# Optimization experiments

Measured on AMD Instinct MI355X. Metric: run time of the kernel, lower is better.

## Reference

```python
import jax, jax.numpy as jnp
import numpy as np
import math

HID = 128
NH = 8
HD = HID // NH
NL = 3
CLIP = 10.0
EPS = 1e-5

def _ln(x, g, b):
    mu = jnp.mean(x, axis=-1, keepdims=True)
    var = jnp.var(x, axis=-1, keepdims=True)
    return (x - mu) * jax.lax.rsqrt(var + EPS) * g + b

def _layer(h, e_bias1, e_gate2, g1, b1, wh, g2, b2, w1, w2):
    B, N, _ = h.shape
    h_in = h
    hn = _ln(h, g1, b1)
    qkv = hn @ wh                                   # (B,N,3H)
    q, k, v = jnp.split(qkv, 3, axis=-1)
    q = q.reshape(B, N, NH, HD).transpose(0, 2, 1, 3)  # (B,nh,N,hd)
    k = k.reshape(B, N, NH, HD).transpose(0, 2, 1, 3)
    v = v.reshape(B, N, NH, HD).transpose(0, 2, 1, 3)
    att = jnp.einsum('bhid,bhjd->bhij', q, k) * (1.0 / math.sqrt(HD))
    att = jax.nn.softmax(att + e_bias1, axis=-1) * e_gate2
    y = jnp.einsum('bhij,bhjd->bhid', att, v)
    y = y.transpose(0, 2, 1, 3).reshape(B, N, HID)
    z = _ln(y + h_in, g2, b2)
    mlp = jax.nn.relu(z @ w1) @ w2
    return mlp + y

def setup_inputs() -> dict:
    key = jax.random.key(0)
    ks = jax.random.split(key, 9)
    d = {
        'node_features': jax.random.normal(ks[0], (16, 256, 2), jnp.float32),
        'edge_features': jax.random.normal(ks[1], (16, 256, 256, 1), jnp.float32),
        'Wn': jax.random.normal(ks[2], (2, HID), jnp.float32) * 0.5,
        'We_in': jax.random.normal(ks[3], (1, HID), jnp.float32) * 0.1,
        'ln1_g': jnp.ones((NL, HID), jnp.float32),
        'ln1_b': jnp.zeros((NL, HID), jnp.float32),
        'Wh': jax.random.normal(ks[4], (NL, HID, 3 * HID), jnp.float32) * (1.0 / math.sqrt(HID)),
        'We': jax.random.normal(ks[5], (NL, HID, 2 * NH), jnp.float32) * (1.0 / math.sqrt(HID)),
        'ln2_g': jnp.ones((NL, HID), jnp.float32),
        'ln2_b': jnp.zeros((NL, HID), jnp.float32),
        'W1': jax.random.normal(ks[6], (NL, HID, 4 * HID), jnp.float32) * (1.0 / math.sqrt(HID)),
        'W2': jax.random.normal(ks[7], (NL, 4 * HID, HID), jnp.float32) * (1.0 / math.sqrt(4 * HID)),
        'Wdec': jax.random.normal(ks[8], (HID, 1), jnp.float32) * (1.0 / math.sqrt(HID)),
    }
    return d

def reference(node_features, edge_features, Wn, We_in, ln1_g, ln1_b, Wh, We, ln2_g, ln2_b, W1, W2, Wdec):
    h = node_features @ Wn                              # (B,N,H)
    e = edge_features @ We_in                           # (B,N,N,H)
    for i in range(NL):
        ee = e @ We[i]                                  # (B,N,N,2*nh)
        ee = ee.transpose(0, 3, 1, 2)                   # (B,2*nh,N,N)
        e1, e2 = ee[:, :NH], ee[:, NH:]
        h = _layer(h, e1, e2, ln1_g[i], ln1_b[i], Wh[i], ln2_g[i], ln2_b[i], W1[i], W2[i])
    out = h @ Wdec                                      # (B,N,1)
    out = CLIP * jnp.tanh(out / math.sqrt(HID))
    return out
```

## Files before the change

### kernel.cpp

```cpp
#include <hip/hip_runtime.h>
#include <math.h>

#define HID 128
#define NHEAD 8
#define NL 3
#define NS 256
#define ROWS 4096

typedef __attribute__((ext_vector_type(8))) short bf16x8;
typedef __attribute__((ext_vector_type(4))) float f32x4;

__device__ __forceinline__ float us2f(unsigned short s) { return __uint_as_float(((unsigned)s) << 16); }
__device__ __forceinline__ unsigned short f2b(float f) {
    unsigned u = __float_as_uint(f);
    return (unsigned short)((u + 0x7fff + ((u >> 16) & 1)) >> 16);
}

__global__ __launch_bounds__(256) void k_prep(
    const float* __restrict__ Wh, const float* __restrict__ W1, const float* __restrict__ W2,
    const float* __restrict__ We_in, const float* __restrict__ We,
    const float* __restrict__ nf, const float* __restrict__ Wn,
    const float* __restrict__ ln1g, const float* __restrict__ ln1b,
    unsigned short* __restrict__ WhH, unsigned short* __restrict__ WhL,
    unsigned short* __restrict__ W1H, unsigned short* __restrict__ W1L,
    unsigned short* __restrict__ W2H, unsigned short* __restrict__ W2L,
    unsigned short* __restrict__ AH, unsigned short* __restrict__ AL,
    float* __restrict__ sbuf, float* __restrict__ h)
{
    int b = blockIdx.x, t = threadIdx.x;
    if (b >= 529) {
        int idx4 = (b - 529) * 256 + t;
        int r = idx4 >> 5, c4 = (idx4 & 31) * 4;
        float n0 = nf[2 * r], n1 = nf[2 * r + 1];
        float4 w0 = *(const float4*)&Wn[c4];
        float4 w1 = *(const float4*)&Wn[HID + c4];
        float v[4] = {n0 * w0.x + n1 * w1.x, n0 * w0.y + n1 * w1.y,
                      n0 * w0.z + n1 * w1.z, n0 * w0.w + n1 * w1.w};
        *(float4*)&h[idx4 * 4] = *(float4*)v;
        float s = v[0] + v[1] + v[2] + v[3];
        float s2 = v[0]*v[0] + v[1]*v[1] + v[2]*v[2] + v[3]*v[3];
        s  += __shfl_xor(s, 1);  s  += __shfl_xor(s, 2);  s  += __shfl_xor(s, 4);
        s  += __shfl_xor(s, 8);  s  += __shfl_xor(s, 16);
        s2 += __shfl_xor(s2, 1); s2 += __shfl_xor(s2, 2); s2 += __shfl_xor(s2, 4);
        s2 += __shfl_xor(s2, 8); s2 += __shfl_xor(s2, 16);
        float mu  = s * (1.f / HID);
        float var = s2 * (1.f / HID) - mu * mu;
        float inv = rsqrtf(var + 1e-5f);
        unsigned short hi4[4], lo4[4];
#pragma unroll
        for (int j = 0; j < 4; ++j) {
            int c = c4 + j;
            float o = (v[j] - mu) * inv * ln1g[c] + ln1b[c];
            hi4[j] = f2b(o); lo4[j] = f2b(o - us2f(hi4[j]));
        }
        *(uint2*)&AH[(long)r * HID + c4] = *(const uint2*)hi4;
        *(uint2*)&AL[(long)r * HID + c4] = *(const uint2*)lo4;
        return;
    }
    if (b == 528) {
        if (t < NL * 2 * NHEAD) {
            int l = t / (2 * NHEAD), j = t % (2 * NHEAD);
            float acc = 0.f;
            for (int c = 0; c < HID; ++c)
                acc += We_in[c] * We[(long)(l * HID + c) * (2 * NHEAD) + j];
            sbuf[t] = acc;
        }
        return;
    }
    const float* S; unsigned short *OH, *OL; int K, N, kt, nt;
    if (b < 144) {
        int l = b / 48, rem = b % 48; kt = rem & 3; nt = rem >> 2; K = 128; N = 384;
        S = Wh + (long)l * 128 * 384; OH = WhH + (long)l * 384 * 128; OL = WhL + (long)l * 384 * 128;
    } else if (b < 336) {
        int b2 = b - 144; int l = b2 / 64, rem = b2 % 64; kt = rem & 3; nt = rem >> 2; K = 128; N = 512;
        S = W1 + (long)l * 128 * 512; OH = W1H + (long)l * 512 * 128; OL = W1L + (long)l * 512 * 128;
    } else {
        int b2 = b - 336; int l = b2 / 64, rem = b2 % 64; kt = rem & 15; nt = rem >> 4; K = 512; N = 128;
        S = W2 + (long)l * 512 * 128; OH = W2H + (long)l * 128 * 512; OL = W2L + (long)l * 128 * 512;
    }
    __shared__ float sm[32][33];
    int i0 = t >> 5, j = t & 31;
#pragma unroll
    for (int p = 0; p < 4; ++p) {
        int i = i0 + p * 8;
        sm[i][j] = S[(long)(kt * 32 + i) * N + nt * 32 + j];
    }
    __syncthreads();
#pragma unroll
    for (int p = 0; p < 4; ++p) {
        int n = i0 + p * 8;
        float v = sm[j][n];
        unsigned short hh = f2b(v);
        long o = (long)(nt * 32 + n) * K + kt * 32 + j;
        OH[o] = hh; OL[o] = f2b(v - us2f(hh));
    }
}

__global__ __launch_bounds__(256) void k_fgemm(
    const unsigned short* __restrict__ AH, const unsigned short* __restrict__ AL,
    const unsigned short* __restrict__ WH, const unsigned short* __restrict__ WL,
    unsigned short* __restrict__ Ch, unsigned short* __restrict__ Cl)
{
    __shared__ unsigned short sAh[64 * 136], sAl[64 * 136];
    __shared__ unsigned short sWh[64 * 136], sWl[64 * 136];
    int t = threadIdx.x;
    int row0 = blockIdx.y * 64, col0 = blockIdx.x * 64;

#pragma unroll
    for (int p = 0; p < 4; ++p) {
        int rr = (t >> 4) + p * 16, ck = t & 15;
        *(uint4*)&sWh[rr * 136 + ck * 8] = *(const uint4*)&WH[(long)(col0 + rr) * 128 + ck * 8];
        *(uint4*)&sWl[rr * 136 + ck * 8] = *(const uint4*)&WL[(long)(col0 + rr) * 128 + ck * 8];
        *(uint4*)&sAh[rr * 136 + ck * 8] = *(const uint4*)&AH[(long)(row0 + rr) * 128 + ck * 8];
        *(uint4*)&sAl[rr * 136 + ck * 8] = *(const uint4*)&AL[(long)(row0 + rr) * 128 + ck * 8];
    }
    __syncthreads();

    int w = t >> 6, lane = t & 63;
    int m = lane & 15, quad = lane >> 4;
    f32x4 acc[4];
#pragma unroll
    for (int i = 0; i < 4; ++i) acc[i] = (f32x4){0.f, 0.f, 0.f, 0.f};
#pragma unroll
    for (int c = 0; c < 4; ++c) {
        bf16x8 ah = *(const bf16x8*)&sAh[(w * 16 + m) * 136 + c * 32 + quad * 8];
        bf16x8 al = *(const bf16x8*)&sAl[(w * 16 + m) * 136 + c * 32 + quad * 8];
#pragma unroll
        for (int nt = 0; nt < 4; ++nt) {
            bf16x8 wh = *(const bf16x8*)&sWh[(nt * 16 + m) * 136 + c * 32 + quad * 8];
            bf16x8 wl = *(const bf16x8*)&sWl[(nt * 16 + m) * 136 + c * 32 + quad * 8];
            acc[nt] = __builtin_amdgcn_mfma_f32_16x16x32_bf16(ah, wh, acc[nt], 0, 0, 0);
            acc[nt] = __builtin_amdgcn_mfma_f32_16x16x32_bf16(ah, wl, acc[nt], 0, 0, 0);
            acc[nt] = __builtin_amdgcn_mfma_f32_16x16x32_bf16(al, wh, acc[nt], 0, 0, 0);
        }
    }
#pragma unroll
    for (int nt = 0; nt < 4; ++nt) {
        unsigned short hi4[4], lo4[4];
#pragma unroll
        for (int r = 0; r < 4; ++r) {
            float v = acc[nt][r];
            hi4[r] = f2b(v); lo4[r] = f2b(v - us2f(hi4[r]));
        }
        long o = (long)(col0 + nt * 16 + m) * ROWS + row0 + w * 16 + quad * 4;
        *(uint2*)&Ch[o] = *(const uint2*)hi4;
        *(uint2*)&Cl[o] = *(const uint2*)lo4;
    }
}

__global__ __launch_bounds__(512, 1) void k_mlp(
    const float* __restrict__ y, const float* __restrict__ h,
    const float* __restrict__ g, const float* __restrict__ b,
    const float* __restrict__ lng, const float* __restrict__ lnb,
    const unsigned short* __restrict__ W1H_, const unsigned short* __restrict__ W1L_,
    const unsigned short* __restrict__ W2H_, const unsigned short* __restrict__ W2L_,
    float* __restrict__ hout,
    unsigned short* __restrict__ AHo, unsigned short* __restrict__ ALo,
    const float* __restrict__ Wdec, float* __restrict__ out)
{
    __shared__ __align__(16) unsigned short sAh[16 * 136], sAl[16 * 136];
    __shared__ __align__(16) unsigned short sHh[16 * 520], sHl[16 * 520];
    int t = threadIdx.x;
    int row0 = blockIdx.x * 16;
    int w = t >> 6, lane = t & 63;
    int m = lane & 15, quad = lane >> 4;

    const unsigned short* w1h = W1H_ + (long)(w * 64 + m) * 128 + quad * 8;
    const unsigned short* w1l = W1L_ + (long)(w * 64 + m) * 128 + quad * 8;
    bf16x8 p1h[4], p1l[4];
#pragma unroll
    for (int nt = 0; nt < 4; ++nt) {
        p1h[nt] = *(const bf16x8*)&w1h[nt * 16 * 128];
        p1l[nt] = *(const bf16x8*)&w1l[nt * 16 * 128];
    }

    {
        int row = t >> 5, cb = (t & 31) * 4;
        float4 a4 = *(const float4*)&y[(long)(row0 + row) * HID + cb];
        float4 b4 = *(const float4*)&h[(long)(row0 + row) * HID + cb];
        float v[4] = {a4.x + b4.x, a4.y + b4.y, a4.z + b4.z, a4.w + b4.w};
        float s = v[0] + v[1] + v[2] + v[3];
        float s2 = v[0]*v[0] + v[1]*v[1] + v[2]*v[2] + v[3]*v[3];
        s  += __shfl_xor(s, 1);  s  += __shfl_xor(s, 2);  s  += __shfl_xor(s, 4);
        s  += __shfl_xor(s, 8);  s  += __shfl_xor(s, 16);
        s2 += __shfl_xor(s2, 1); s2 += __shfl_xor(s2, 2); s2 += __shfl_xor(s2, 4);
        s2 += __shfl_xor(s2, 8); s2 += __shfl_xor(s2, 16);
        float mu  = s * (1.f / HID);
        float var = s2 * (1.f / HID) - mu * mu;
        float inv = rsqrtf(var + 1e-5f);
        unsigned short hi4[4], lo4[4];
#pragma unroll
        for (int j = 0; j < 4; ++j) {
            int c = cb + j;
            float o = (v[j] - mu) * inv * g[c] + b[c];
            hi4[j] = f2b(o); lo4[j] = f2b(o - us2f(hi4[j]));
        }
        *(uint2*)&sAh[row * 136 + cb] = *(const uint2*)hi4;
        *(uint2*)&sAl[row * 136 + cb] = *(const uint2*)lo4;
    }
    __syncthreads();

    f32x4 acc1[4];
#pragma unroll
    for (int i = 0; i < 4; ++i) acc1[i] = (f32x4){0.f, 0.f, 0.f, 0.f};
#pragma unroll
    for (int c = 0; c < 4; ++c) {
        bf16x8 ah = *(const bf16x8*)&sAh[m * 136 + c * 32 + quad * 8];
        bf16x8 al = *(const bf16x8*)&sAl[m * 136 + c * 32 + quad * 8];
#pragma unroll
        for (int nt = 0; nt < 4; ++nt) {
            bf16x8 wh = (c == 0) ? p1h[nt] : *(const bf16x8*)&w1h[nt * 16 * 128 + c * 32];
            bf16x8 wl = (c == 0) ? p1l[nt] : *(const bf16x8*)&w1l[nt * 16 * 128 + c * 32];
            acc1[nt] = __builtin_amdgcn_mfma_f32_16x16x32_bf16(wh, ah, acc1[nt], 0, 0, 0);
            acc1[nt] = __builtin_amdgcn_mfma_f32_16x16x32_bf16(wh, al, acc1[nt], 0, 0, 0);
            acc1[nt] = __builtin_amdgcn_mfma_f32_16x16x32_bf16(wl, ah, acc1[nt], 0, 0, 0);
        }
    }
#pragma unroll
    for (int nt = 0; nt < 4; ++nt) {
        unsigned short hi4[4], lo4[4];
#pragma unroll
        for (int r = 0; r < 4; ++r) {
            float v = fmaxf(acc1[nt][r], 0.f);
            hi4[r] = f2b(v);
            lo4[r] = f2b(v - us2f(hi4[r]));
        }
        int kk = w * 64 + nt * 16 + quad * 4;
        *(uint2*)&sHh[m * 520 + kk] = *(const uint2*)hi4;
        *(uint2*)&sHl[m * 520 + kk] = *(const uint2*)lo4;
    }

    const unsigned short* w2h = W2H_ + (long)(w * 16 + m) * 512 + quad * 8;
    const unsigned short* w2l = W2L_ + (long)(w * 16 + m) * 512 + quad * 8;
    bf16x8 p2h = *(const bf16x8*)w2h;
    bf16x8 p2l = *(const bf16x8*)w2l;
    __syncthreads();

    f32x4 acc2 = (f32x4){0.f, 0.f, 0.f, 0.f};
#pragma unroll
    for (int c = 0; c < 16; ++c) {
        bf16x8 ah = *(const bf16x8*)&sHh[m * 520 + c * 32 + quad * 8];
        bf16x8 al = *(const bf16x8*)&sHl[m * 520 + c * 32 + quad * 8];
        bf16x8 wh = (c == 0) ? p2h : *(const bf16x8*)&w2h[c * 32];
        bf16x8 wl = (c == 0) ? p2l : *(const bf16x8*)&w2l[c * 32];
        acc2 = __builtin_amdgcn_mfma_f32_16x16x32_bf16(ah, wh, acc2, 0, 0, 0);
        acc2 = __builtin_amdgcn_mfma_f32_16x16x32_bf16(ah, wl, acc2, 0, 0, 0);
        acc2 = __builtin_amdgcn_mfma_f32_16x16x32_bf16(al, wh, acc2, 0, 0, 0);
    }
    __syncthreads();
    float* ht = (float*)&sHh[0];
#pragma unroll
    for (int r = 0; r < 4; ++r) {
        int row = quad * 4 + r;
        int col = w * 16 + m;
        float v = acc2[r] + y[(long)(row0 + row) * HID + col];
        hout[(long)(row0 + row) * HID + col] = v;
        ht[row * 132 + col] = v;
    }
    __syncthreads();
    if (Wdec) {
        if (t < 256) {
            int row = t >> 4, sub = t & 15;
            float vv[8];
            *(float4*)&vv[0] = *(const float4*)&ht[row * 132 + sub * 8];
            *(float4*)&vv[4] = *(const float4*)&ht[row * 132 + sub * 8 + 4];
            float a = 0.f;
#pragma unroll
            for (int j = 0; j < 8; ++j) a += vv[j] * Wdec[sub * 8 + j];
            a += __shfl_xor(a, 1); a += __shfl_xor(a, 2); a += __shfl_xor(a, 4); a += __shfl_xor(a, 8);
            if (sub == 0) out[row0 + row] = 10.f * tanhf(a * 0.08838834764831845f);
        }
    } else {
        int row = t >> 5, cb = (t & 31) * 4;
        float v[4];
        v[0] = ht[row * 132 + cb];     v[1] = ht[row * 132 + cb + 1];
        v[2] = ht[row * 132 + cb + 2]; v[3] = ht[row * 132 + cb + 3];
        float s = v[0] + v[1] + v[2] + v[3];
        float s2 = v[0]*v[0] + v[1]*v[1] + v[2]*v[2] + v[3]*v[3];
        s  += __shfl_xor(s, 1);  s  += __shfl_xor(s, 2);  s  += __shfl_xor(s, 4);
        s  += __shfl_xor(s, 8);  s  += __shfl_xor(s, 16);
        s2 += __shfl_xor(s2, 1); s2 += __shfl_xor(s2, 2); s2 += __shfl_xor(s2, 4);
        s2 += __shfl_xor(s2, 8); s2 += __shfl_xor(s2, 16);
        float mu  = s * (1.f / HID);
        float var = s2 * (1.f / HID) - mu * mu;
        float inv = rsqrtf(var + 1e-5f);
        unsigned short hi4[4], lo4[4];
#pragma unroll
        for (int j = 0; j < 4; ++j) {
            int c = cb + j;
            float o = (v[j] - mu) * inv * lng[c] + lnb[c];
            hi4[j] = f2b(o); lo4[j] = f2b(o - us2f(hi4[j]));
        }
        *(uint2*)&AHo[(long)(row0 + row) * HID + cb] = *(const uint2*)hi4;
        *(uint2*)&ALo[(long)(row0 + row) * HID + cb] = *(const uint2*)lo4;
    }
}

#define PAS 268
#define KQS 20
__global__ __launch_bounds__(256) void k_attn(
    const unsigned short* __restrict__ qkvH, const unsigned short* __restrict__ qkvL,
    const float* __restrict__ ef, const float* __restrict__ sbuf,
    int layer, float* __restrict__ y)
{
    __shared__ unsigned short Kh[NS * KQS], Kl[NS * KQS];
    __shared__ unsigned short Qh[64 * KQS], Ql[64 * KQS];
    __shared__ unsigned short Vh[16 * PAS], Vl[16 * PAS];
    __shared__ unsigned short Pa[4][16 * PAS];
    int bid = blockIdx.x;
    int q4 = bid & 3, hh = (bid >> 2) & 7, bb = bid >> 5;
    int t = threadIdx.x;
    {
        int d = t >> 4, kc = (t & 15) * 16;
        long base = (long)ROWS * (HID + hh * 16 + d) + bb * NS + kc;
        long vbase = base + (long)ROWS * 128;
        union { uint4 u[2]; unsigned short s[16]; } KH, KL, VH, VL;
        KH.u[0] = *(const uint4*)&qkvH[base];      KH.u[1] = *(const uint4*)&qkvH[base + 8];
        KL.u[0] = *(const uint4*)&qkvL[base];      KL.u[1] = *(const uint4*)&qkvL[base + 8];
        VH.u[0] = *(const uint4*)&qkvH[vbase];     VH.u[1] = *(const uint4*)&qkvH[vbase + 8];
        VL.u[0] = *(const uint4*)&qkvL[vbase];     VL.u[1] = *(const uint4*)&qkvL[vbase + 8];
#pragma unroll
        for (int j = 0; j < 16; ++j) {
            Kh[(kc + j) * KQS + d] = KH.s[j];
            Kl[(kc + j) * KQS + d] = KL.s[j];
        }
#pragma unroll
        for (int j = 0; j < 4; ++j) {
            *(uint2*)&Vh[d * PAS + kc + j * 4] = *(const uint2*)&VH.s[j * 4];
            *(uint2*)&Vl[d * PAS + kc + j * 4] = *(const uint2*)&VL.s[j * 4];
        }
    }
    {
        int d = t >> 4, rc = (t & 15) * 4;
        long qb = (long)ROWS * (hh * 16 + d) + bb * NS + q4 * 64 + rc;
        union { uint2 u; unsigned short s[4]; } QH, QL;
        QH.u = *(const uint2*)&qkvH[qb];
        QL.u = *(const uint2*)&qkvL[qb];
#pragma unroll
        for (int j = 0; j < 4; ++j) {
            Qh[(rc + j) * KQS + d] = QH.s[j];
            Ql[(rc + j) * KQS + d] = QL.s[j];
        }
    }
    __syncthreads();
    int w = t >> 6, lane = t & 63;
    int m = lane & 15, quad = lane >> 4;
    float s1  = sbuf[layer * 16 + hh];
    float s2g = sbuf[layer * 16 + NHEAD + hh];
    unsigned short* Paw = Pa[w];

    bf16x8 qh = (bf16x8){0,0,0,0,0,0,0,0}, ql = qh;
    if (quad < 2) {
        qh = *(const bf16x8*)&Qh[(w * 16 + m) * KQS + quad * 8];
        ql = *(const bf16x8*)&Ql[(w * 16 + m) * KQS + quad * 8];
    }
    f32x4 sc[16];
#pragma unroll
    for (int ct = 0; ct < 16; ++ct) {
        bf16x8 kh = (bf16x8){0,0,0,0,0,0,0,0}, kl = kh;
        if (quad < 2) {
            kh = *(const bf16x8*)&Kh[(ct * 16 + m) * KQS + quad * 8];
            kl = *(const bf16x8*)&Kl[(ct * 16 + m) * KQS + quad * 8];
        }
        f32x4 a = (f32x4){0.f, 0.f, 0.f, 0.f};
        a = __builtin_amdgcn_mfma_f32_16x16x32_bf16(qh, kh, a, 0, 0, 0);
        a = __builtin_amdgcn_mfma_f32_16x16x32_bf16(qh, kl, a, 0, 0, 0);
        a = __builtin_amdgcn_mfma_f32_16x16x32_bf16(ql, kh, a, 0, 0, 0);
        sc[ct] = a;
    }
    int baserow = q4 * 64 + w * 16 + quad * 4;
    float s[4] = {0.f, 0.f, 0.f, 0.f};
#pragma unroll
    for (int ct = 0; ct < 16; ++ct) {
#pragma unroll
        for (int r = 0; r < 4; ++r) {
            float e = ef[((long)(bb * NS + baserow + r)) * NS + ct * 16 + m];
            float p = __expf(sc[ct][r] * 0.25f + e * s1);
            s[r] += p;
            Paw[(quad * 4 + r) * PAS + ct * 16 + m] = f2b(p * e);
        }
    }
    float inv[4];
#pragma unroll
    for (int r = 0; r < 4; ++r) {
        float ss = s[r];
        ss += __shfl_xor(ss, 1); ss += __shfl_xor(ss, 2);
        ss += __shfl_xor(ss, 4); ss += __shfl_xor(ss, 8);
        inv[r] = s2g / ss;
    }
    f32x4 acc = (f32x4){0.f, 0.f, 0.f, 0.f};
#pragma unroll
    for (int sft = 0; sft < 8; ++sft) {
        bf16x8 pf = *(const bf16x8*)&Paw[m * PAS + sft * 32 + quad * 8];
        bf16x8 vh = *(const bf16x8*)&Vh[m * PAS + sft * 32 + quad * 8];
        bf16x8 vl = *(const bf16x8*)&Vl[m * PAS + sft * 32 + quad * 8];
        acc = __builtin_amdgcn_mfma_f32_16x16x32_bf16(pf, vh, acc, 0, 0, 0);
        acc = __builtin_amdgcn_mfma_f32_16x16x32_bf16(pf, vl, acc, 0, 0, 0);
    }
#pragma unroll
    for (int r = 0; r < 4; ++r) {
        int row = q4 * 64 + w * 16 + quad * 4 + r;
        y[((long)(bb * NS + row)) * HID + hh * 16 + m] = acc[r] * inv[r];
    }
}

extern "C" void kernel_launch(void* const* d_in, const int* in_sizes, int n_in,
                              void* d_out, int out_size, void* d_ws, size_t ws_size,
                              hipStream_t stream) {
    const float* nf    = (const float*)d_in[0];
    const float* ef    = (const float*)d_in[1];
    const float* Wn    = (const float*)d_in[2];
    const float* We_in = (const float*)d_in[3];
    const float* ln1g  = (const float*)d_in[4];
    const float* ln1b  = (const float*)d_in[5];
    const float* Wh    = (const float*)d_in[6];
    const float* We    = (const float*)d_in[7];
    const float* ln2g  = (const float*)d_in[8];
    const float* ln2b  = (const float*)d_in[9];
    const float* W1    = (const float*)d_in[10];
    const float* W2    = (const float*)d_in[11];
    const float* Wdec  = (const float*)d_in[12];

    float* ws   = (float*)d_ws;
    float* sbuf = ws;
    float* h    = ws + 64;
    float* y    = h + ROWS * HID;
    unsigned short* qkvH = (unsigned short*)(y + ROWS * HID);
    unsigned short* qkvL = qkvH + (long)384 * ROWS;
    unsigned short* WhH  = qkvL + (long)384 * ROWS;
    unsigned short* WhL  = WhH + (long)NL * 384 * 128;
    unsigned short* W1H  = WhL + (long)NL * 384 * 128;
    unsigned short* W1L  = W1H + (long)NL * 512 * 128;
    unsigned short* W2H  = W1L + (long)NL * 512 * 128;
    unsigned short* W2L  = W2H + (long)NL * 128 * 512;
    unsigned short* AH   = W2L + (long)NL * 128 * 512;
    unsigned short* AL   = AH + (long)ROWS * HID;

    k_prep<<<529 + ROWS * HID / 1024, 256, 0, stream>>>(Wh, W1, W2, We_in, We, nf, Wn,
                                    ln1g, ln1b,
                                    WhH, WhL, W1H, W1L, W2H, W2L, AH, AL, sbuf, h);
    for (int l = 0; l < NL; ++l) {
        k_fgemm<<<dim3(6, 64), 256, 0, stream>>>(AH, AL,
            WhH + (long)l * 384 * 128, WhL + (long)l * 384 * 128,
            qkvH, qkvL);
        k_attn<<<512, 256, 0, stream>>>(qkvH, qkvL, ef, sbuf, l, y);
        int last = (l == NL - 1);
        k_mlp<<<ROWS / 16, 512, 0, stream>>>(y, h,
            ln2g + l * HID, ln2b + l * HID,
            ln1g + (last ? 0 : (l + 1) * HID), ln1b + (last ? 0 : (l + 1) * HID),
            W1H + (long)l * 512 * 128, W1L + (long)l * 512 * 128,
            W2H + (long)l * 128 * 512, W2L + (long)l * 128 * 512,
            h, AH, AL, last ? Wdec : nullptr, (float*)d_out);
    }
}
```

Baseline: 200.9 us.

## Fuse next-layer QKV projection into MLP kernel epilogue

The MLP kernel now applies the next layer's LayerNorm into shared memory and immediately computes the QKV projection with split-bf16 MFMA, writing qkvH/qkvL directly. This removes two of the three separate k_fgemm launches and the AH/AL round trip through global memory. The trade-off is more work and register pressure in the MLP kernel, with each block re-reading the Wh weights from global memory.

Measured after the change: 203.1 us. About the same (+1.1%).

```diff
diff --git a/kernel.cpp b/kernel.cpp
--- a/kernel.cpp
+++ b/kernel.cpp
@@ -154,8 +154,9 @@
     const float* __restrict__ lng, const float* __restrict__ lnb,
     const unsigned short* __restrict__ W1H_, const unsigned short* __restrict__ W1L_,
     const unsigned short* __restrict__ W2H_, const unsigned short* __restrict__ W2L_,
+    const unsigned short* __restrict__ WhHn, const unsigned short* __restrict__ WhLn,
     float* __restrict__ hout,
-    unsigned short* __restrict__ AHo, unsigned short* __restrict__ ALo,
+    unsigned short* __restrict__ qkvH, unsigned short* __restrict__ qkvL,
     const float* __restrict__ Wdec, float* __restrict__ out)
 {
     __shared__ __align__(16) unsigned short sAh[16 * 136], sAl[16 * 136];
@@ -271,28 +272,66 @@
             if (sub == 0) out[row0 + row] = 10.f * tanhf(a * 0.08838834764831845f);
         }
     } else {
-        int row = t >> 5, cb = (t & 31) * 4;
-        float v[4];
-        v[0] = ht[row * 132 + cb];     v[1] = ht[row * 132 + cb + 1];
-        v[2] = ht[row * 132 + cb + 2]; v[3] = ht[row * 132 + cb + 3];
-        float s = v[0] + v[1] + v[2] + v[3];
-        float s2 = v[0]*v[0] + v[1]*v[1] + v[2]*v[2] + v[3]*v[3];
-        s  += __shfl_xor(s, 1);  s  += __shfl_xor(s, 2);  s  += __shfl_xor(s, 4);
-        s  += __shfl_xor(s, 8);  s  += __shfl_xor(s, 16);
-        s2 += __shfl_xor(s2, 1); s2 += __shfl_xor(s2, 2); s2 += __shfl_xor(s2, 4);
-        s2 += __shfl_xor(s2, 8); s2 += __shfl_xor(s2, 16);
-        float mu  = s * (1.f / HID);
-        float var = s2 * (1.f / HID) - mu * mu;
-        float inv = rsqrtf(var + 1e-5f);
-        unsigned short hi4[4], lo4[4];
-#pragma unroll
-        for (int j = 0; j < 4; ++j) {
-            int c = cb + j;
-            float o = (v[j] - mu) * inv * lng[c] + lnb[c];
-            hi4[j] = f2b(o); lo4[j] = f2b(o - us2f(hi4[j]));
-        }
-        *(uint2*)&AHo[(long)(row0 + row) * HID + cb] = *(const uint2*)hi4;
-        *(uint2*)&ALo[(long)(row0 + row) * HID + cb] = *(const uint2*)lo4;
+        const unsigned short* whn = WhHn + (long)(w * 48 + m) * 128 + quad * 8;
+        const unsigned short* wln = WhLn + (long)(w * 48 + m) * 128 + quad * 8;
+        bf16x8 pqh[3], pql[3];
+#pragma unroll
+        for (int nt = 0; nt < 3; ++nt) {
+            pqh[nt] = *(const bf16x8*)&whn[nt * 16 * 128];
+            pql[nt] = *(const bf16x8*)&wln[nt * 16 * 128];
+        }
+        {
+            int row = t >> 5, cb = (t & 31) * 4;
+            float v[4];
+            *(float4*)v = *(const float4*)&ht[row * 132 + cb];
+            float s = v[0] + v[1] + v[2] + v[3];
+            float s2 = v[0]*v[0] + v[1]*v[1] + v[2]*v[2] + v[3]*v[3];
+            s  += __shfl_xor(s, 1);  s  += __shfl_xor(s, 2);  s  += __shfl_xor(s, 4);
+            s  += __shfl_xor(s, 8);  s  += __shfl_xor(s, 16);
+            s2 += __shfl_xor(s2, 1); s2 += __shfl_xor(s2, 2); s2 += __shfl_xor(s2, 4);
+            s2 += __shfl_xor(s2, 8); s2 += __shfl_xor(s2, 16);
+            float mu  = s * (1.f / HID);
+            float var = s2 * (1.f / HID) - mu * mu;
+            float inv = rsqrtf(var + 1e-5f);
+            unsigned short hi4[4], lo4[4];
+#pragma unroll
+            for (int j = 0; j < 4; ++j) {
+                int c = cb + j;
+                float o = (v[j] - mu) * inv * lng[c] + lnb[c];
+                hi4[j] = f2b(o); lo4[j] = f2b(o - us2f(hi4[j]));
+            }
+            *(uint2*)&sAh[row * 136 + cb] = *(const uint2*)hi4;
+            *(uint2*)&sAl[row * 136 + cb] = *(const uint2*)lo4;
+        }
+        __syncthreads();
+        f32x4 aq[3];
+#pragma unroll
+        for (int i = 0; i < 3; ++i) aq[i] = (f32x4){0.f, 0.f, 0.f, 0.f};
+#pragma unroll
+        for (int c = 0; c < 4; ++c) {
+            bf16x8 ah = *(const bf16x8*)&sAh[m * 136 + c * 32 + quad * 8];
+            bf16x8 al = *(const bf16x8*)&sAl[m * 136 + c * 32 + quad * 8];
+#pragma unroll
+            for (int nt = 0; nt < 3; ++nt) {
+                bf16x8 wh = (c == 0) ? pqh[nt] : *(const bf16x8*)&whn[nt * 16 * 128 + c * 32];
+                bf16x8 wl = (c == 0) ? pql[nt] : *(const bf16x8*)&wln[nt * 16 * 128 + c * 32];
+                aq[nt] = __builtin_amdgcn_mfma_f32_16x16x32_bf16(ah, wh, aq[nt], 0, 0, 0);
+                aq[nt] = __builtin_amdgcn_mfma_f32_16x16x32_bf16(ah, wl, aq[nt], 0, 0, 0);
+                aq[nt] = __builtin_amdgcn_mfma_f32_16x16x32_bf16(al, wh, aq[nt], 0, 0, 0);
+            }
+        }
+#pragma unroll
+        for (int nt = 0; nt < 3; ++nt) {
+            unsigned short hi4[4], lo4[4];
+#pragma unroll
+            for (int r = 0; r < 4; ++r) {
+                float v = aq[nt][r];
+                hi4[r] = f2b(v); lo4[r] = f2b(v - us2f(hi4[r]));
+            }
+            long o = (long)(w * 48 + nt * 16 + m) * ROWS + row0 + quad * 4;
+            *(uint2*)&qkvH[o] = *(const uint2*)hi4;
+            *(uint2*)&qkvL[o] = *(const uint2*)lo4;
+        }
     }
 }
 
@@ -439,10 +478,8 @@
     k_prep<<<529 + ROWS * HID / 1024, 256, 0, stream>>>(Wh, W1, W2, We_in, We, nf, Wn,
                                     ln1g, ln1b,
                                     WhH, WhL, W1H, W1L, W2H, W2L, AH, AL, sbuf, h);
+    k_fgemm<<<dim3(6, 64), 256, 0, stream>>>(AH, AL, WhH, WhL, qkvH, qkvL);
     for (int l = 0; l < NL; ++l) {
-        k_fgemm<<<dim3(6, 64), 256, 0, stream>>>(AH, AL,
-            WhH + (long)l * 384 * 128, WhL + (long)l * 384 * 128,
-            qkvH, qkvL);
         k_attn<<<512, 256, 0, stream>>>(qkvH, qkvL, ef, sbuf, l, y);
         int last = (l == NL - 1);
         k_mlp<<<ROWS / 16, 512, 0, stream>>>(y, h,
@@ -450,6 +487,8 @@
             ln1g + (last ? 0 : (l + 1) * HID), ln1b + (last ? 0 : (l + 1) * HID),
             W1H + (long)l * 512 * 128, W1L + (long)l * 512 * 128,
             W2H + (long)l * 128 * 512, W2L + (long)l * 128 * 512,
-            h, AH, AL, last ? Wdec : nullptr, (float*)d_out);
-    }
-}
+            WhH + (long)(last ? 0 : (l + 1)) * 384 * 128,
+            WhL + (long)(last ? 0 : (l + 1)) * 384 * 128,
+            h, qkvH, qkvL, last ? Wdec : nullptr, (float*)d_out);
+    }
+}
```
